# Performance work log

Hardware: AMD Instinct MI355X
Metric: run time of the kernel (lower is better)

## Reference

```python
import jax, jax.numpy as jnp
import numpy as np

H = 4          # num attention heads
LRELU = 0.2    # DGL GATConv leaky-relu slope
N_GT, N_AG = 100000, 20000
E_GT, E_COMM = 640000, 320000
D_GT, D_AG = 32, 64
VIS, COMM, MSG, OUT = 64, 128, 64, 5
NUM_COMM_STEPS = 2


def _leaky(x):
    return jnp.where(x >= 0, x, LRELU * x)


def gat(feat_src, feat_dst, w_src, w_dst, a_l, a_r, bias, src, dst, n_dst, dh):
    """Bipartite DGL GATConv: residual=Identity (in_dst == H*dh), activation=ReLU."""
    fs = (feat_src @ w_src).reshape(-1, H, dh)   # [Ns,H,dh]
    fd = (feat_dst @ w_dst).reshape(-1, H, dh)   # [Nd,H,dh]
    el = (fs * a_l[None]).sum(-1)                # [Ns,H]
    er = (fd * a_r[None]).sum(-1)                # [Nd,H]
    e = _leaky(el[src] + er[dst])                # [E,H]
    emax = jax.ops.segment_max(e, dst, num_segments=n_dst)
    ex = jnp.exp(e - emax[dst])
    denom = jax.ops.segment_sum(ex, dst, num_segments=n_dst)
    a = ex / denom[dst]                          # edge softmax over in-edges
    rst = jax.ops.segment_sum(fs[src] * a[..., None], dst, num_segments=n_dst)
    rst = rst + feat_dst.reshape(n_dst, H, dh)   # identity residual
    rst = rst + bias.reshape(1, H, dh)
    return jax.nn.relu(rst).reshape(n_dst, H * dh)


def gru(x, h, w_ih, w_hh, b_ih, b_hh):
    gi = x @ w_ih + b_ih
    gh = h @ w_hh + b_hh
    i_r, i_z, i_n = jnp.split(gi, 3, axis=1)
    h_r, h_z, h_n = jnp.split(gh, 3, axis=1)
    r = jax.nn.sigmoid(i_r + h_r)
    zg = jax.nn.sigmoid(i_z + h_z)
    n = jnp.tanh(i_n + r * h_n)
    return (1.0 - zg) * n + zg * h


def setup_inputs() -> dict:
    key = jax.random.key(0)
    ks = jax.random.split(key, 32)
    def w(k, shp):
        return (jax.random.normal(k, shp, dtype=jnp.float32) / np.sqrt(shp[0])).astype(jnp.float32)
    dh1, dh2 = VIS // H, COMM // H
    inp = {
        'feat_gt': jax.random.normal(ks[0], (N_GT, D_GT), dtype=jnp.float32),
        'feat_agent': jax.random.normal(ks[1], (N_AG, D_AG), dtype=jnp.float32),
        'z': jax.random.normal(ks[2], (N_AG, COMM), dtype=jnp.float32),
        'gt_src': jax.random.randint(ks[3], (E_GT,), 0, N_GT, dtype=jnp.int32),
        'gt_dst': jax.random.randint(ks[4], (E_GT,), 0, N_AG, dtype=jnp.int32),
        'comm_src': jax.random.randint(ks[5], (E_COMM,), 0, N_AG, dtype=jnp.int32),
        'comm_dst': jax.random.randint(ks[6], (E_COMM,), 0, N_AG, dtype=jnp.int32),
        # vis1 GATConv (gt->agent), out 64 = 4 heads x 16
        'w1_src': w(ks[7], (D_GT, VIS)), 'w1_dst': w(ks[8], (D_AG, VIS)),
        'a1_l': w(ks[9], (H, dh1)), 'a1_r': w(ks[10], (H, dh1)),
        'b1': jnp.zeros((VIS,), jnp.float32),
        'w2_src': w(ks[11], (D_GT, COMM)), 'w2_dst': w(ks[12], (VIS + D_AG, COMM)),
        'a2_l': w(ks[13], (H, dh2)), 'a2_r': w(ks[14], (H, dh2)),
        'b2': jnp.zeros((COMM,), jnp.float32),
        # comm f_enc: mlp([128,128,64]) with ReLU everywhere
        'enc_w1': w(ks[15], (COMM, 128)), 'enc_b1': jnp.zeros((128,), jnp.float32),
        'enc_w2': w(ks[16], (128, MSG)), 'enc_b2': jnp.zeros((MSG,), jnp.float32),
        # GRUCell(in=COMM+MSG=192, hidden=COMM=128), stored [in, 3*hidden]
        'gru_w_ih': w(ks[17], (COMM + MSG, 3 * COMM)),
        'gru_w_hh': w(ks[18], (COMM, 3 * COMM)),
        'gru_b_ih': jnp.zeros((3 * COMM,), jnp.float32),
        'gru_b_hh': jnp.zeros((3 * COMM,), jnp.float32),
        # f_out
        'out_w': w(ks[19], (COMM, OUT)), 'out_b': jnp.zeros((OUT,), jnp.float32),
    }
    return inp


def _forward(feat_gt, feat_agent, z, gt_src, gt_dst, comm_src, comm_dst,
             w1_src, w1_dst, a1_l, a1_r, b1,
             w2_src, w2_dst, a2_l, a2_r, b2,
             enc_w1, enc_b1, enc_w2, enc_b2,
             gru_w_ih, gru_w_hh, gru_b_ih, gru_b_hh,
             out_w, out_b):
    n_ag = feat_agent.shape[0]
    h_vis1 = gat(feat_gt, feat_agent, w1_src, w1_dst, a1_l, a1_r, b1,
                 gt_src, gt_dst, n_ag, VIS // H)
    dst2 = jnp.concatenate([h_vis1, feat_agent], axis=1)
    h = gat(feat_gt, dst2, w2_src, w2_dst, a2_l, a2_r, b2,
            gt_src, gt_dst, n_ag, COMM // H)
    deg = jax.ops.segment_sum(jnp.ones_like(comm_dst, dtype=jnp.float32),
                              comm_dst, num_segments=n_ag)
    denom = jnp.maximum(deg, 1.0)[:, None]
    zz = z
    for _ in range(NUM_COMM_STEPS):
        m = jax.nn.relu(jax.nn.relu(h @ enc_w1 + enc_b1) @ enc_w2 + enc_b2)  # per-node f_enc
        y = jax.ops.segment_sum(m[comm_src], comm_dst, num_segments=n_ag) / denom  # mailbox mean
        h = gru(jnp.concatenate([h, y], axis=1), zz, gru_w_ih, gru_w_hh, gru_b_ih, gru_b_hh)
        zz = h
    h_out = h @ out_w + out_b
    return h_out, zz


def reference(feat_gt, feat_agent, z, gt_src, gt_dst, comm_src, comm_dst,
              w1_src, w1_dst, a1_l, a1_r, b1,
              w2_src, w2_dst, a2_l, a2_r, b2,
              enc_w1, enc_b1, enc_w2, enc_b2,
              gru_w_ih, gru_w_hh, gru_b_ih, gru_b_hh,
              out_w, out_b):
    return _forward(feat_gt, feat_agent, z, gt_src, gt_dst, comm_src, comm_dst,
                    w1_src, w1_dst, a1_l, a1_r, b1,
                    w2_src, w2_dst, a2_l, a2_r, b2,
                    enc_w1, enc_b1, enc_w2, enc_b2,
                    gru_w_ih, gru_w_hh, gru_b_ih, gru_b_hh,
                    out_w, out_b)
```

## Files before the change

### kernel.cpp

```cpp
#include <hip/hip_runtime.h>
#include <math.h>

#define NHEAD 4
#define LRELU_S 0.2f
constexpr int N_GT = 100000, N_AG = 20000;
constexpr int E_GT = 640000, E_COMM = 320000;
constexpr int OUTD = 5;
constexpr int NBLK_SC = (N_AG + 255) / 256;
constexpr int MB_GT = (N_GT + 63) / 64;
constexpr int FS_TILES = 3 * MB_GT;
constexpr int ETILES  = (N_AG + 31) / 32;
constexpr int GGROUPS = (N_AG + 3) / 4;

constexpr long O_CNTP_GT = 0;
constexpr long O_CNTP_CM = 320000;
constexpr long O_FSB1    = 0;
constexpr long O_FSB2    = 3200000;
constexpr long O_EL1     = 12800000;
constexpr long O_EL2     = 13200000;
constexpr long O_ER1     = 14880000;
constexpr long O_RST2    = 17600000;
constexpr long O_DINV    = 20160000;
constexpr long O_OFFS_GT = 20180000;
constexpr long O_SRT_GT  = 20200004;
constexpr long O_OFFS_CM = 20840004;
constexpr long O_SRT_CM  = 20860008;
constexpr long O_PART    = 21180008;
constexpr long O_V       = 21220008;
constexpr long O_WB      = 21300000;
constexpr long O_RANK_GT = 21500000;
constexpr long O_RANK_CM = 22140000;
constexpr long O_M  = 10240000;

constexpr long WB_FS  = 0;
constexpr long WB_E1  = 6144;
constexpr long WB_E2  = 22528;
constexpr long WB_RZ  = 30720;
constexpr long WB_GIN = 112640;
constexpr long WB_GHN = 137216;

using bf8      = __attribute__((ext_vector_type(8))) short;
using f32x4v   = __attribute__((ext_vector_type(4))) float;
using ushort8v = __attribute__((ext_vector_type(8))) unsigned short;

__device__ __forceinline__ unsigned short f2bf(float x) {
    unsigned u = __float_as_uint(x);
    u += 0x7FFFu + ((u >> 16) & 1u);
    return (unsigned short)(u >> 16);
}
__device__ __forceinline__ float bf2f(unsigned short u) {
    return __uint_as_float(((unsigned)u) << 16);
}

__global__ __launch_bounds__(256) void p0_k(
    const float* __restrict__ w1s, const float* __restrict__ w1d,
    const float* __restrict__ a1l, const float* __restrict__ a1r,
    const float* __restrict__ w2s, const float* __restrict__ w2d,
    const float* __restrict__ a2l, const float* __restrict__ a2r,
    const float* __restrict__ e1, const float* __restrict__ e2,
    const float* __restrict__ gih, const float* __restrict__ ghh,
    float* __restrict__ ws)
{
    const int tid = (int)(blockIdx.x * 256 + threadIdx.x);
    const int NT  = (int)(gridDim.x * 256);
    unsigned* wsu = reinterpret_cast<unsigned*>(ws);
    unsigned short* wb = reinterpret_cast<unsigned short*>(ws + O_WB);
    for (int i = tid; i < 640000; i += NT) wsu[O_CNTP_GT + i] = 0u;
    for (int i = tid; i < 153600; i += NT) {
        float val;
        if (i < 2048)        { long l = i;          long n = l / 32,  k = l % 32;  val = w1s[k * 64 + n]; }
        else if (i < 6144)   { long l = i - 2048;   long n = l / 32,  k = l % 32;  val = w2s[k * 128 + n]; }
        else if (i < 22528)  { long l = i - 6144;   long n = l / 128, k = l % 128; val = e1[k * 128 + n]; }
        else if (i < 30720)  { long l = i - 22528;  long n = l / 128, k = l % 128; val = e2[k * 64 + n]; }
        else if (i < 112640) { long l = i - 30720;  long n = l / 320, k = l % 320;
                               val = (k < 192) ? gih[k * 384 + n] : ghh[(k - 192) * 384 + n]; }
        else if (i < 137216) { long l = i - 112640; long n = l / 192, k = l % 192; val = gih[k * 384 + 256 + n]; }
        else                 { long l = i - 137216; long n = l / 128, k = l % 128; val = ghh[k * 384 + 256 + n]; }
        wb[i] = f2bf(val);
    }
    if (tid < 1024) {
        const int i = tid;
        const float *wp, *ap; int dh, local;
        if (i < 128)      { wp = w1s; ap = a1l; dh = 16; local = i; }
        else if (i < 384) { wp = w1d; ap = a1r; dh = 16; local = i - 128; }
        else if (i < 512) { wp = w2s; ap = a2l; dh = 32; local = i - 384; }
        else              { wp = w2d; ap = a2r; dh = 32; local = i - 512; }
        int k = local >> 2, hh = local & 3;
        float s = 0.f;
        for (int j = 0; j < dh; ++j) s += wp[k * (4 * dh) + hh * dh + j] * ap[hh * dh + j];
        ws[O_V + i] = s;
    }
}

__global__ __launch_bounds__(256) void p1_k(
    const int* __restrict__ gt_dst, const int* __restrict__ comm_dst,
    const float* __restrict__ feat_gt, const float* __restrict__ feat_agent,
    float* __restrict__ ws)
{
    const int tid = (int)(blockIdx.x * 256 + threadIdx.x);
    unsigned* wsu = reinterpret_cast<unsigned*>(ws);
    if (tid < E_GT) {
        wsu[O_RANK_GT + tid] = atomicAdd(wsu + O_CNTP_GT + (long)gt_dst[tid] * 16, 1u);
    } else if (tid < E_GT + E_COMM) {
        int j = tid - E_GT;
        wsu[O_RANK_CM + j] = atomicAdd(wsu + O_CNTP_CM + (long)comm_dst[j] * 16, 1u);
    }
    const float* v1  = ws + O_V;
    const float* v2  = ws + O_V + 384;
    const float* vr1 = ws + O_V + 128;
    float* el1 = ws + O_EL1;
    float* el2 = ws + O_EL2;
    float* er1 = ws + O_ER1;
    if (tid < N_GT) {
        const int i = tid;
        float a[8] = {};
        const float* fp = feat_gt + (long)i * 32;
        for (int k = 0; k < 32; ++k) {
            float x = fp[k];
#pragma unroll
            for (int j = 0; j < 4; ++j) a[j] += x * v1[4 * k + j];
#pragma unroll
            for (int j = 0; j < 4; ++j) a[4 + j] += x * v2[4 * k + j];
        }
        *reinterpret_cast<float4*>(el1 + 4l * i) = {a[0], a[1], a[2], a[3]};
        *reinterpret_cast<float4*>(el2 + 4l * i) = {a[4], a[5], a[6], a[7]};
    } else if (tid < N_GT + N_AG) {
        int r = tid - N_GT;
        float a0 = 0, a1 = 0, a2 = 0, a3 = 0;
        const float* fp = feat_agent + (long)r * 64;
        for (int k = 0; k < 64; ++k) {
            float x = fp[k];
            a0 += x * vr1[4 * k];     a1 += x * vr1[4 * k + 1];
            a2 += x * vr1[4 * k + 2]; a3 += x * vr1[4 * k + 3];
        }
        *reinterpret_cast<float4*>(er1 + 4l * r) = {a0, a1, a2, a3};
    }
}

__global__ __launch_bounds__(256) void p2_k(float* __restrict__ ws)
{
    __shared__ unsigned shu[256];
    unsigned* wsu = reinterpret_cast<unsigned*>(ws);
    const int b = (int)blockIdx.x, t = (int)threadIdx.x;
    const int g  = (b >= NBLK_SC) ? 1 : 0;
    const int cb = b - g * NBLK_SC;
    const int i  = cb * 256 + t;
    const unsigned* cnt = wsu + (g ? O_CNTP_CM : O_CNTP_GT);
    unsigned c = (i < N_AG) ? cnt[(long)i * 16] : 0u;
    if (g && i < N_AG) ws[O_DINV + i] = 1.0f / fmaxf((float)c, 1.0f);
    shu[t] = c;
    __syncthreads();
    for (int off = 1; off < 256; off <<= 1) {
        unsigned v = (t >= off) ? shu[t - off] : 0u;
        __syncthreads();
        shu[t] += v;
        __syncthreads();
    }
    unsigned* offs = wsu + (g ? O_OFFS_CM : O_OFFS_GT);
    if (i < N_AG) offs[i] = shu[t] - c;
    if (t == 255) wsu[O_PART + b] = shu[255];
}

__global__ __launch_bounds__(256) void p3_k(float* __restrict__ ws)
{
    __shared__ unsigned shu[128];
    unsigned* wsu = reinterpret_cast<unsigned*>(ws);
    const int b = (int)blockIdx.x, t = (int)threadIdx.x;
    const int g  = (b >= NBLK_SC) ? 1 : 0;
    const int cb = b - g * NBLK_SC;
    if (t < 128) shu[t] = (t < cb) ? wsu[O_PART + g * NBLK_SC + t] : 0u;
    __syncthreads();
    for (int off = 64; off >= 1; off >>= 1) {
        if (t < off) shu[t] += shu[t + off];
        __syncthreads();
    }
    const unsigned pre = shu[0];
    unsigned* offs = wsu + (g ? O_OFFS_CM : O_OFFS_GT);
    const int i = cb * 256 + t;
    if (i < N_AG) offs[i] += pre;
    if (b == NBLK_SC - 1 && t == 0)     wsu[O_OFFS_GT + N_AG] = E_GT;
    if (b == 2 * NBLK_SC - 1 && t == 0) wsu[O_OFFS_CM + N_AG] = E_COMM;
}

__global__ __launch_bounds__(256) void p4_k(
    const int* __restrict__ gt_src, const int* __restrict__ gt_dst,
    const int* __restrict__ comm_src, const int* __restrict__ comm_dst,
    const float* __restrict__ A, float* __restrict__ ws)
{
    unsigned* wsu = reinterpret_cast<unsigned*>(ws);
    const int t = (int)threadIdx.x;
    const int tid = (int)(blockIdx.x * 256 + t);
    if (tid < E_GT) {
        wsu[O_SRT_GT + wsu[O_OFFS_GT + gt_dst[tid]] + wsu[O_RANK_GT + tid]] = (unsigned)gt_src[tid];
    } else if (tid < E_GT + E_COMM) {
        int j = tid - E_GT;
        wsu[O_SRT_CM + wsu[O_OFFS_CM + comm_dst[j]] + wsu[O_RANK_CM + j]] = (unsigned)comm_src[j];
    }

    __shared__ __align__(16) unsigned short As[64][40];
    __shared__ __align__(16) unsigned short Bs[64][40];
    const unsigned short* Btc = reinterpret_cast<unsigned short*>(ws + O_WB) + WB_FS;
    unsigned short* fsb1 = reinterpret_cast<unsigned short*>(ws + O_FSB1);
    unsigned short* fsb2 = reinterpret_cast<unsigned short*>(ws + O_FSB2);
    const int lane = t & 63, wv = t >> 6;
    const int wm = wv & 1, wn = wv >> 1;
    const int quad = lane >> 4, l16 = lane & 15;
    const int rA = t >> 3, cA = (t & 7) * 4;
    const int rB = t >> 2, cB = (t & 3) * 8;
    const int tt = (int)blockIdx.x;
    if (tt >= FS_TILES) return;
    const int n0 = (tt % 3) * 64, m0 = (tt / 3) * 64;
#pragma unroll
    for (int half = 0; half < 2; ++half) {
        const int r = rA + half * 32;
        const int row = m0 + r;
        float4 v = {0.f, 0.f, 0.f, 0.f};
        if (row < N_GT) v = *reinterpret_cast<const float4*>(A + (long)row * 32 + cA);
        ushort4 bb;
        bb.x = f2bf(v.x); bb.y = f2bf(v.y); bb.z = f2bf(v.z); bb.w = f2bf(v.w);
        *reinterpret_cast<ushort4*>(&As[r][cA]) = bb;
    }
    *reinterpret_cast<ushort8v*>(&Bs[rB][cB]) =
        *reinterpret_cast<const ushort8v*>(Btc + (long)(n0 + rB) * 32 + cB);
    __syncthreads();
    f32x4v acc[2][2] = {};
    const bf8 a0 = *reinterpret_cast<const bf8*>(&As[wm * 32 + l16][quad * 8]);
    const bf8 a1 = *reinterpret_cast<const bf8*>(&As[wm * 32 + 16 + l16][quad * 8]);
    const bf8 b0v = *reinterpret_cast<const bf8*>(&Bs[wn * 32 + l16][quad * 8]);
    const bf8 b1v = *reinterpret_cast<const bf8*>(&Bs[wn * 32 + 16 + l16][quad * 8]);
    acc[0][0] = __builtin_amdgcn_mfma_f32_16x16x32_bf16(a0, b0v, acc[0][0], 0, 0, 0);
    acc[0][1] = __builtin_amdgcn_mfma_f32_16x16x32_bf16(a0, b1v, acc[0][1], 0, 0, 0);
    acc[1][0] = __builtin_amdgcn_mfma_f32_16x16x32_bf16(a1, b0v, acc[1][0], 0, 0, 0);
    acc[1][1] = __builtin_amdgcn_mfma_f32_16x16x32_bf16(a1, b1v, acc[1][1], 0, 0, 0);
#pragma unroll
    for (int mt = 0; mt < 2; ++mt)
#pragma unroll
        for (int nt = 0; nt < 2; ++nt)
#pragma unroll
            for (int r = 0; r < 4; ++r) {
                const int row = m0 + wm * 32 + mt * 16 + quad * 4 + r;
                const int col = n0 + wn * 32 + nt * 16 + l16;
                if (row < N_GT) {
                    unsigned short v16 = f2bf(acc[mt][nt][r]);
                    if (col < 64) fsb1[(long)row * 64 + col] = v16;
                    else          fsb2[(long)row * 128 + (col - 64)] = v16;
                }
            }
}

__global__ __launch_bounds__(256) void gat12_k(
    const unsigned* __restrict__ offs, const unsigned* __restrict__ ssrc,
    const float* __restrict__ el1, const float* __restrict__ er1,
    const float* __restrict__ el2,
    const unsigned short* __restrict__ fsb1, const unsigned short* __restrict__ fsb2,
    const float* __restrict__ feat_agent,
    const float* __restrict__ b1, const float* __restrict__ b2,
    const float* __restrict__ vr2, float* __restrict__ out)
{
    const int wid = threadIdx.x >> 6, lane = threadIdx.x & 63;
    const int d = blockIdx.x * 4 + wid;
    if (d >= N_AG) return;
    const int h = lane >> 4, ei = lane & 15;
    const unsigned beg = __builtin_amdgcn_readfirstlane(offs[d]);
    const unsigned end = __builtin_amdgcn_readfirstlane(offs[d + 1]);
    const unsigned smax = (unsigned)N_GT - 1u;

    float s = 0.f, acc0 = 0.f;
    {
        const float er_h = er1[4l * d + h];
        for (unsigned base = beg; base < end; base += 16) {
            const unsigned na = min(16u, end - base);
            unsigned sv = ssrc[base + ((unsigned)ei < na ? (unsigned)ei : 0u)];
            sv = min(sv, smax);
            float p = 0.f;
            if ((unsigned)ei < na) {
                float x = el1[4l * sv + h] + er_h;
                x = (x >= 0.f) ? x : LRELU_S * x;
                p = __expf(x);
            }
            unsigned short fw[16];
#pragma unroll
            for (int j = 0; j < 16; ++j) {
                const unsigned sj = min(ssrc[min(base + (unsigned)j, end - 1u)], smax);
                fw[j] = fsb1[(long)sj * 64 + lane];
            }
#pragma unroll
            for (int j = 0; j < 16; ++j) {
                const float pj = __shfl(p, (h << 4) | j);
                s += pj;
                acc0 += pj * bf2f(fw[j]);
            }
        }
    }
    const float inv1 = (s > 0.f) ? 1.f / s : 0.f;
    const float r1 = feat_agent[(long)d * 64 + lane];
    const float o = fmaxf(acc0 * inv1 + r1 + b1[lane], 0.f);

    float e0 = o * vr2[lane * 4 + 0] + r1 * vr2[(64 + lane) * 4 + 0];
    float e1v = o * vr2[lane * 4 + 1] + r1 * vr2[(64 + lane) * 4 + 1];
    float e2v = o * vr2[lane * 4 + 2] + r1 * vr2[(64 + lane) * 4 + 2];
    float e3v = o * vr2[lane * 4 + 3] + r1 * vr2[(64 + lane) * 4 + 3];
#pragma unroll
    for (int off = 1; off < 64; off <<= 1) {
        e0  += __shfl_xor(e0, off);
        e1v += __shfl_xor(e1v, off);
        e2v += __shfl_xor(e2v, off);
        e3v += __shfl_xor(e3v, off);
    }
    const float er_h2 = (h == 0) ? e0 : (h == 1) ? e1v : (h == 2) ? e2v : e3v;

    const int c0 = lane * 2;
    float s2 = 0.f, A0 = 0.f, A1 = 0.f;
    for (unsigned base = beg; base < end; base += 16) {
        const unsigned na = min(16u, end - base);
        unsigned sv = ssrc[base + ((unsigned)ei < na ? (unsigned)ei : 0u)];
        sv = min(sv, smax);
        float p = 0.f;
        if ((unsigned)ei < na) {
            float x = el2[4l * sv + h] + er_h2;
            x = (x >= 0.f) ? x : LRELU_S * x;
            p = __expf(x);
        }
        unsigned fw[16];
#pragma unroll
        for (int j = 0; j < 16; ++j) {
            const unsigned sj = min(ssrc[min(base + (unsigned)j, end - 1u)], smax);
            fw[j] = *reinterpret_cast<const unsigned*>(fsb2 + (long)sj * 128 + c0);
        }
#pragma unroll
        for (int j = 0; j < 16; ++j) {
            const float pj = __shfl(p, (h << 4) | j);
            s2 += pj;
            A0 += pj * __uint_as_float((fw[j] & 0xFFFFu) << 16);
            A1 += pj * __uint_as_float((fw[j] >> 16) << 16);
        }
    }
    const float inv2 = (s2 > 0.f) ? 1.f / s2 : 0.f;
    const float rox = __shfl(o, c0 & 63);
    const float roy = __shfl(o, (c0 + 1) & 63);
    float2 r;
    if (c0 < 64) { r.x = rox; r.y = roy; }
    else r = *reinterpret_cast<const float2*>(feat_agent + (long)d * 64 + (c0 - 64));
    float2 oo;
    oo.x = fmaxf(A0 * inv2 + r.x + b2[c0], 0.f);
    oo.y = fmaxf(A1 * inv2 + r.y + b2[c0 + 1], 0.f);
    *reinterpret_cast<float2*>(out + (long)d * 128 + c0) = oo;
}

__global__ __launch_bounds__(512) void enc_k(
    const float* __restrict__ h,
    const unsigned short* __restrict__ we1, const unsigned short* __restrict__ we2,
    const float* __restrict__ eb1, const float* __restrict__ eb2,
    unsigned short* __restrict__ mb)
{
    __shared__ __align__(16) unsigned short As[32][136];
    __shared__ __align__(16) unsigned short Ts[32][136];
    const int tid = (int)threadIdx.x;
    const int lane = tid & 63, w = tid >> 6;
    const int quad = lane >> 4, l16 = lane & 15;
    const int m0 = (int)blockIdx.x * 32;
#pragma unroll
    for (int it = 0; it < 2; ++it) {
        int idx = tid + it * 512;
        int row = idx >> 5, cc = (idx & 31) * 4;
        int grow = m0 + row;
        float4 v = {0.f, 0.f, 0.f, 0.f};
        if (grow < N_AG) v = *reinterpret_cast<const float4*>(h + (long)grow * 128 + cc);
        ushort4 b;
        b.x = f2bf(v.x); b.y = f2bf(v.y); b.z = f2bf(v.z); b.w = f2bf(v.w);
        *reinterpret_cast<ushort4*>(&As[row][cc]) = b;
    }
    __syncthreads();
    {
        const int j0 = w * 16;
        const unsigned short* p = we1 + (long)(j0 + l16) * 128 + quad * 8;
        bf8 bw[4];
#pragma unroll
        for (int i = 0; i < 4; ++i) bw[i] = *reinterpret_cast<const bf8*>(p + i * 32);
        f32x4v acc[2] = {};
#pragma unroll
        for (int i = 0; i < 4; ++i) {
            const int k0 = i * 32;
            const bf8 a0 = *reinterpret_cast<const bf8*>(&As[l16][k0 + quad * 8]);
            const bf8 a1 = *reinterpret_cast<const bf8*>(&As[16 + l16][k0 + quad * 8]);
            acc[0] = __builtin_amdgcn_mfma_f32_16x16x32_bf16(a0, bw[i], acc[0], 0, 0, 0);
            acc[1] = __builtin_amdgcn_mfma_f32_16x16x32_bf16(a1, bw[i], acc[1], 0, 0, 0);
        }
        const int j = j0 + l16;
        const float bj = eb1[j];
#pragma unroll
        for (int mt = 0; mt < 2; ++mt)
#pragma unroll
            for (int r = 0; r < 4; ++r)
                Ts[mt * 16 + quad * 4 + r][j] = f2bf(fmaxf(acc[mt][r] + bj, 0.f));
    }
    __syncthreads();
    if (w < 4) {
        const int j0 = w * 16;
        const unsigned short* p = we2 + (long)(j0 + l16) * 128 + quad * 8;
        bf8 bw[4];
#pragma unroll
        for (int i = 0; i < 4; ++i) bw[i] = *reinterpret_cast<const bf8*>(p + i * 32);
        f32x4v acc[2] = {};
#pragma unroll
        for (int i = 0; i < 4; ++i) {
            const int k0 = i * 32;
            const bf8 a0 = *reinterpret_cast<const bf8*>(&Ts[l16][k0 + quad * 8]);
            const bf8 a1 = *reinterpret_cast<const bf8*>(&Ts[16 + l16][k0 + quad * 8]);
            acc[0] = __builtin_amdgcn_mfma_f32_16x16x32_bf16(a0, bw[i], acc[0], 0, 0, 0);
            acc[1] = __builtin_amdgcn_mfma_f32_16x16x32_bf16(a1, bw[i], acc[1], 0, 0, 0);
        }
        const int j = j0 + l16;
        const float bj = eb2[j];
#pragma unroll
        for (int mt = 0; mt < 2; ++mt)
#pragma unroll
            for (int r = 0; r < 4; ++r) {
                const int row = m0 + mt * 16 + quad * 4 + r;
                if (row < N_AG)
                    mb[(long)row * 64 + j] = f2bf(fmaxf(acc[mt][r] + bj, 0.f));
            }
    }
}

__global__ __launch_bounds__(512) void gru_k(
    const float* __restrict__ h_in,
    const unsigned* __restrict__ coffs, const unsigned* __restrict__ cssrc,
    const unsigned short* __restrict__ mbx, const float* __restrict__ dinv,
    const float* zz,
    const unsigned short* __restrict__ wrz, const unsigned short* __restrict__ wgin,
    const unsigned short* __restrict__ wghn,
    const float* __restrict__ gbih, const float* __restrict__ gbhh,
    float* hout,
    const float* __restrict__ ow, const float* __restrict__ ob, float* __restrict__ outp)
{
    __shared__ __align__(16) unsigned short As[32][328];
    __shared__ __align__(16) float Ys[32][64];
    const int tid = (int)threadIdx.x;
    const int lane = tid & 63, w = tid >> 6;
    const int quad = lane >> 4, l16 = lane & 15;
    const int m0 = (int)blockIdx.x * 32;

    {
        const unsigned smax = (unsigned)N_AG - 1u;
#pragma unroll 1
        for (int q = 0; q < 4; ++q) {
            const int d = m0 + w * 4 + q;
            const unsigned beg  = __builtin_amdgcn_readfirstlane(coffs[d]);
            const unsigned endo = __builtin_amdgcn_readfirstlane(coffs[d + 1]);
            float acc = 0.f;
            for (unsigned base = beg; base < endo; base += 32) {
                const unsigned na = min(32u, endo - base);
                unsigned short fw[32];
#pragma unroll
                for (int j = 0; j < 32; ++j) {
                    const unsigned sj = min(cssrc[min(base + (unsigned)j, endo - 1u)], smax);
                    fw[j] = mbx[(long)sj * 64 + lane];
                }
#pragma unroll
                for (int j = 0; j < 32; ++j)
                    if ((unsigned)j < na) acc += bf2f(fw[j]);
            }
            Ys[w * 4 + q][lane] = acc * dinv[d];
        }
    }
    __syncthreads();

#pragma unroll
    for (int it = 0; it < 5; ++it) {
        int idx = tid + it * 512;
        int row = idx / 80, cc = (idx - row * 80) * 4;
        int grow = m0 + row;
        float4 v = {0.f, 0.f, 0.f, 0.f};
        if (grow < N_AG) {
            if (cc < 128)      v = *reinterpret_cast<const float4*>(h_in + (long)grow * 128 + cc);
            else if (cc < 192) v = *reinterpret_cast<const float4*>(&Ys[row][cc - 128]);
            else               v = *reinterpret_cast<const float4*>(zz + (long)grow * 128 + (cc - 192));
        }
        ushort4 b;
        b.x = f2bf(v.x); b.y = f2bf(v.y); b.z = f2bf(v.z); b.w = f2bf(v.w);
        *reinterpret_cast<ushort4*>(&As[row][cc]) = b;
    }
    __syncthreads();

    f32x4v aR[2] = {}, aZ[2] = {}, aI[2] = {}, aH[2] = {};
    const int j0 = w * 16;
    const unsigned short* pR = wrz + (long)(j0 + l16) * 320 + quad * 8;
    const unsigned short* pZ = wrz + (long)(128 + j0 + l16) * 320 + quad * 8;
#pragma unroll
    for (int half = 0; half < 2; ++half) {
        bf8 bR[5], bZ[5];
#pragma unroll
        for (int i = 0; i < 5; ++i) {
            const int k0 = half * 160 + i * 32;
            bR[i] = *reinterpret_cast<const bf8*>(pR + k0);
            bZ[i] = *reinterpret_cast<const bf8*>(pZ + k0);
        }
#pragma unroll
        for (int i = 0; i < 5; ++i) {
            const int k0 = half * 160 + i * 32;
            const bf8 a0 = *reinterpret_cast<const bf8*>(&As[l16][k0 + quad * 8]);
            const bf8 a1 = *reinterpret_cast<const bf8*>(&As[16 + l16][k0 + quad * 8]);
            aR[0] = __builtin_amdgcn_mfma_f32_16x16x32_bf16(a0, bR[i], aR[0], 0, 0, 0);
            aR[1] = __builtin_amdgcn_mfma_f32_16x16x32_bf16(a1, bR[i], aR[1], 0, 0, 0);
            aZ[0] = __builtin_amdgcn_mfma_f32_16x16x32_bf16(a0, bZ[i], aZ[0], 0, 0, 0);
            aZ[1] = __builtin_amdgcn_mfma_f32_16x16x32_bf16(a1, bZ[i], aZ[1], 0, 0, 0);
        }
    }
    {
        const unsigned short* pI = wgin + (long)(j0 + l16) * 192 + quad * 8;
        bf8 bI[6];
#pragma unroll
        for (int i = 0; i < 6; ++i) bI[i] = *reinterpret_cast<const bf8*>(pI + i * 32);
#pragma unroll
        for (int i = 0; i < 6; ++i) {
            const int k0 = i * 32;
            const bf8 a0 = *reinterpret_cast<const bf8*>(&As[l16][k0 + quad * 8]);
            const bf8 a1 = *reinterpret_cast<const bf8*>(&As[16 + l16][k0 + quad * 8]);
            aI[0] = __builtin_amdgcn_mfma_f32_16x16x32_bf16(a0, bI[i], aI[0], 0, 0, 0);
            aI[1] = __builtin_amdgcn_mfma_f32_16x16x32_bf16(a1, bI[i], aI[1], 0, 0, 0);
        }
    }
    {
        const unsigned short* pH = wghn + (long)(j0 + l16) * 128 + quad * 8;
        bf8 bH[4];
#pragma unroll
        for (int i = 0; i < 4; ++i) bH[i] = *reinterpret_cast<const bf8*>(pH + i * 32);
#pragma unroll
        for (int i = 0; i < 4; ++i) {
            const int k0 = 192 + i * 32;
            const bf8 a0 = *reinterpret_cast<const bf8*>(&As[l16][k0 + quad * 8]);
            const bf8 a1 = *reinterpret_cast<const bf8*>(&As[16 + l16][k0 + quad * 8]);
            aH[0] = __builtin_amdgcn_mfma_f32_16x16x32_bf16(a0, bH[i], aH[0], 0, 0, 0);
            aH[1] = __builtin_amdgcn_mfma_f32_16x16x32_bf16(a1, bH[i], aH[1], 0, 0, 0);
        }
    }
    const int j = j0 + l16;
    float hv[2][4];
#pragma unroll
    for (int mt = 0; mt < 2; ++mt)
#pragma unroll
        for (int r = 0; r < 4; ++r) {
            const int row = m0 + mt * 16 + quad * 4 + r;
            float v = 0.f;
            if (row < N_AG) {
                const float rr = 1.f / (1.f + __expf(-(aR[mt][r] + gbih[j] + gbhh[j])));
                const float zg = 1.f / (1.f + __expf(-(aZ[mt][r] + gbih[128 + j] + gbhh[128 + j])));
                const float nn = tanhf(aI[mt][r] + gbih[256 + j] + rr * (aH[mt][r] + gbhh[256 + j]));
                const float hp = zz[(long)row * 128 + j];
                v = (1.f - zg) * nn + zg * hp;
            }
            hv[mt][r] = v;
        }

    if (outp == nullptr) {
#pragma unroll
        for (int mt = 0; mt < 2; ++mt)
#pragma unroll
            for (int r = 0; r < 4; ++r) {
                const int row = m0 + mt * 16 + quad * 4 + r;
                if (row < N_AG) hout[(long)row * 128 + j] = hv[mt][r];
            }
    } else {
        __syncthreads();
        float* Hs = reinterpret_cast<float*>(&As[0][0]);
#pragma unroll
        for (int mt = 0; mt < 2; ++mt)
#pragma unroll
            for (int r = 0; r < 4; ++r)
                Hs[(mt * 16 + quad * 4 + r) * 128 + j] = hv[mt][r];
        __syncthreads();
        for (int it = tid; it < 32 * 32; it += 512) {
            const int row = it >> 5, c4 = (it & 31) * 4;
            const float4 v = *reinterpret_cast<const float4*>(&Hs[row * 128 + c4]);
            *reinterpret_cast<float4*>(outp + (long)N_AG * OUTD + (long)(m0 + row) * 128 + c4) = v;
        }
        for (int it = tid; it < 32 * OUTD; it += 512) {
            const int row = it / OUTD, jj = it - row * OUTD;
            float a = ob[jj];
            const float* hr = &Hs[row * 128];
            for (int k = 0; k < 128; ++k) a += hr[k] * ow[k * OUTD + jj];
            outp[(long)(m0 + row) * OUTD + jj] = a;
        }
    }
}

extern "C" void kernel_launch(void* const* d_in, const int* in_sizes, int n_in,
                              void* d_out, int out_size, void* d_ws, size_t ws_size,
                              hipStream_t stream) {
    const float* feat_gt    = (const float*)d_in[0];
    const float* feat_agent = (const float*)d_in[1];
    const float* z_in       = (const float*)d_in[2];
    const int*   gt_src     = (const int*)d_in[3];
    const int*   gt_dst     = (const int*)d_in[4];
    const int*   comm_src   = (const int*)d_in[5];
    const int*   comm_dst   = (const int*)d_in[6];
    const float* w1_src = (const float*)d_in[7];
    const float* w1_dst = (const float*)d_in[8];
    const float* a1_l   = (const float*)d_in[9];
    const float* a1_r   = (const float*)d_in[10];
    const float* b1     = (const float*)d_in[11];
    const float* w2_src = (const float*)d_in[12];
    const float* w2_dst = (const float*)d_in[13];
    const float* a2_l   = (const float*)d_in[14];
    const float* a2_r   = (const float*)d_in[15];
    const float* b2     = (const float*)d_in[16];
    const float* enc_w1 = (const float*)d_in[17];
    const float* enc_b1 = (const float*)d_in[18];
    const float* enc_w2 = (const float*)d_in[19];
    const float* enc_b2 = (const float*)d_in[20];
    const float* gw_ih  = (const float*)d_in[21];
    const float* gw_hh  = (const float*)d_in[22];
    const float* gb_ih  = (const float*)d_in[23];
    const float* gb_hh  = (const float*)d_in[24];
    const float* out_w  = (const float*)d_in[25];
    const float* out_b  = (const float*)d_in[26];

    float* ws = (float*)d_ws;
    unsigned* wsu = (unsigned*)d_ws;
    unsigned short* wb = (unsigned short*)(ws + O_WB);
    float* out = (float*)d_out;

    float* hptr = ws + O_RST2;
    unsigned short* mb = (unsigned short*)(ws + O_M);

    p0_k<<<dim3(2500), dim3(256), 0, stream>>>(w1_src, w1_dst, a1_l, a1_r,
                                               w2_src, w2_dst, a2_l, a2_r,
                                               enc_w1, enc_w2, gw_ih, gw_hh, ws);
    p1_k<<<dim3(3750), dim3(256), 0, stream>>>(gt_dst, comm_dst, feat_gt, feat_agent, ws);
    p2_k<<<dim3(2 * NBLK_SC), dim3(256), 0, stream>>>(ws);
    p3_k<<<dim3(2 * NBLK_SC), dim3(256), 0, stream>>>(ws);
    p4_k<<<dim3(FS_TILES), dim3(256), 0, stream>>>(gt_src, gt_dst, comm_src, comm_dst,
                                                   feat_gt, ws);

    gat12_k<<<dim3(GGROUPS), dim3(256), 0, stream>>>(
        wsu + O_OFFS_GT, wsu + O_SRT_GT,
        ws + O_EL1, ws + O_ER1, ws + O_EL2,
        (const unsigned short*)(ws + O_FSB1), (const unsigned short*)(ws + O_FSB2),
        feat_agent, b1, b2, ws + O_V + 512, hptr);

    for (int step = 0; step < 2; ++step) {
        const float* zz = (step == 0) ? z_in : hptr;
        enc_k<<<dim3(ETILES), dim3(512), 0, stream>>>(hptr, wb + WB_E1, wb + WB_E2,
                                                      enc_b1, enc_b2, mb);
        gru_k<<<dim3(ETILES), dim3(512), 0, stream>>>(hptr,
                                                      wsu + O_OFFS_CM, wsu + O_SRT_CM,
                                                      mb, ws + O_DINV, zz,
                                                      wb + WB_RZ, wb + WB_GIN, wb + WB_GHN,
                                                      gb_ih, gb_hh, hptr,
                                                      (step == 1) ? out_w : nullptr,
                                                      (step == 1) ? out_b : nullptr,
                                                      (step == 1) ? out : nullptr);
    }
}
```

Before: 362.6 us.

## Fuse scan kernels and give each fs GEMM block all three column tiles

The two-pass block scan (p2/p3) becomes a single kernel in which each block recomputes its prefix by summing all earlier counts directly, which removes one launch and the partial-sum buffer. The scatter/GEMM kernel p4 now launches one block per 64-row tile and loops over all three 64-column output tiles. The A tile is loaded once instead of three times, and the edge scatter becomes a grid-stride loop. In exchange, each scan block re-reads up to N_AG strided counts, and p4 runs a third as many blocks with more serial work per block.

```diff
diff --git a/kernel.cpp b/kernel.cpp
--- a/kernel.cpp
+++ b/kernel.cpp
@@ -8,7 +8,6 @@
 constexpr int OUTD = 5;
 constexpr int NBLK_SC = (N_AG + 255) / 256;
 constexpr int MB_GT = (N_GT + 63) / 64;
-constexpr int FS_TILES = 3 * MB_GT;
 constexpr int ETILES  = (N_AG + 31) / 32;
 constexpr int GGROUPS = (N_AG + 3) / 4;
 
@@ -137,15 +136,27 @@
     }
 }
 
-__global__ __launch_bounds__(256) void p2_k(float* __restrict__ ws)
+__global__ __launch_bounds__(256) void p23_k(float* __restrict__ ws)
 {
     __shared__ unsigned shu[256];
     unsigned* wsu = reinterpret_cast<unsigned*>(ws);
     const int b = (int)blockIdx.x, t = (int)threadIdx.x;
     const int g  = (b >= NBLK_SC) ? 1 : 0;
     const int cb = b - g * NBLK_SC;
-    const int i  = cb * 256 + t;
     const unsigned* cnt = wsu + (g ? O_CNTP_CM : O_CNTP_GT);
+
+    unsigned psum = 0u;
+    for (int i = t; i < cb * 256; i += 256) psum += cnt[(long)i * 16];
+    shu[t] = psum;
+    __syncthreads();
+    for (int off = 128; off >= 1; off >>= 1) {
+        if (t < off) shu[t] += shu[t + off];
+        __syncthreads();
+    }
+    const unsigned pre = shu[0];
+    __syncthreads();
+
+    const int i = cb * 256 + t;
     unsigned c = (i < N_AG) ? cnt[(long)i * 16] : 0u;
     if (g && i < N_AG) ws[O_DINV + i] = 1.0f / fmaxf((float)c, 1.0f);
     shu[t] = c;
@@ -157,27 +168,7 @@
         __syncthreads();
     }
     unsigned* offs = wsu + (g ? O_OFFS_CM : O_OFFS_GT);
-    if (i < N_AG) offs[i] = shu[t] - c;
-    if (t == 255) wsu[O_PART + b] = shu[255];
-}
-
-__global__ __launch_bounds__(256) void p3_k(float* __restrict__ ws)
-{
-    __shared__ unsigned shu[128];
-    unsigned* wsu = reinterpret_cast<unsigned*>(ws);
-    const int b = (int)blockIdx.x, t = (int)threadIdx.x;
-    const int g  = (b >= NBLK_SC) ? 1 : 0;
-    const int cb = b - g * NBLK_SC;
-    if (t < 128) shu[t] = (t < cb) ? wsu[O_PART + g * NBLK_SC + t] : 0u;
-    __syncthreads();
-    for (int off = 64; off >= 1; off >>= 1) {
-        if (t < off) shu[t] += shu[t + off];
-        __syncthreads();
-    }
-    const unsigned pre = shu[0];
-    unsigned* offs = wsu + (g ? O_OFFS_CM : O_OFFS_GT);
-    const int i = cb * 256 + t;
-    if (i < N_AG) offs[i] += pre;
+    if (i < N_AG) offs[i] = pre + shu[t] - c;
     if (b == NBLK_SC - 1 && t == 0)     wsu[O_OFFS_GT + N_AG] = E_GT;
     if (b == 2 * NBLK_SC - 1 && t == 0) wsu[O_OFFS_CM + N_AG] = E_COMM;
 }
@@ -189,16 +180,18 @@
 {
     unsigned* wsu = reinterpret_cast<unsigned*>(ws);
     const int t = (int)threadIdx.x;
-    const int tid = (int)(blockIdx.x * 256 + t);
-    if (tid < E_GT) {
-        wsu[O_SRT_GT + wsu[O_OFFS_GT + gt_dst[tid]] + wsu[O_RANK_GT + tid]] = (unsigned)gt_src[tid];
-    } else if (tid < E_GT + E_COMM) {
-        int j = tid - E_GT;
-        wsu[O_SRT_CM + wsu[O_OFFS_CM + comm_dst[j]] + wsu[O_RANK_CM + j]] = (unsigned)comm_src[j];
+    const int NT = (int)(gridDim.x * 256);
+    for (int i = (int)(blockIdx.x * 256 + t); i < E_GT + E_COMM; i += NT) {
+        if (i < E_GT) {
+            wsu[O_SRT_GT + wsu[O_OFFS_GT + gt_dst[i]] + wsu[O_RANK_GT + i]] = (unsigned)gt_src[i];
+        } else {
+            int j = i - E_GT;
+            wsu[O_SRT_CM + wsu[O_OFFS_CM + comm_dst[j]] + wsu[O_RANK_CM + j]] = (unsigned)comm_src[j];
+        }
     }
 
     __shared__ __align__(16) unsigned short As[64][40];
-    __shared__ __align__(16) unsigned short Bs[64][40];
+    __shared__ __align__(16) unsigned short Bs[192][40];
     const unsigned short* Btc = reinterpret_cast<unsigned short*>(ws + O_WB) + WB_FS;
     unsigned short* fsb1 = reinterpret_cast<unsigned short*>(ws + O_FSB1);
     unsigned short* fsb2 = reinterpret_cast<unsigned short*>(ws + O_FSB2);
@@ -206,10 +199,7 @@
     const int wm = wv & 1, wn = wv >> 1;
     const int quad = lane >> 4, l16 = lane & 15;
     const int rA = t >> 3, cA = (t & 7) * 4;
-    const int rB = t >> 2, cB = (t & 3) * 8;
-    const int tt = (int)blockIdx.x;
-    if (tt >= FS_TILES) return;
-    const int n0 = (tt % 3) * 64, m0 = (tt / 3) * 64;
+    const int m0 = (int)blockIdx.x * 64;
 #pragma unroll
     for (int half = 0; half < 2; ++half) {
         const int r = rA + half * 32;
@@ -220,32 +210,41 @@
         bb.x = f2bf(v.x); bb.y = f2bf(v.y); bb.z = f2bf(v.z); bb.w = f2bf(v.w);
         *reinterpret_cast<ushort4*>(&As[r][cA]) = bb;
     }
-    *reinterpret_cast<ushort8v*>(&Bs[rB][cB]) =
-        *reinterpret_cast<const ushort8v*>(Btc + (long)(n0 + rB) * 32 + cB);
-    __syncthreads();
-    f32x4v acc[2][2] = {};
+#pragma unroll
+    for (int it = 0; it < 3; ++it) {
+        const int idx = t + it * 256;
+        const int r = idx >> 2, c8 = (idx & 3) * 8;
+        *reinterpret_cast<ushort8v*>(&Bs[r][c8]) =
+            *reinterpret_cast<const ushort8v*>(Btc + (long)r * 32 + c8);
+    }
+    __syncthreads();
     const bf8 a0 = *reinterpret_cast<const bf8*>(&As[wm * 32 + l16][quad * 8]);
     const bf8 a1 = *reinterpret_cast<const bf8*>(&As[wm * 32 + 16 + l16][quad * 8]);
-    const bf8 b0v = *reinterpret_cast<const bf8*>(&Bs[wn * 32 + l16][quad * 8]);
-    const bf8 b1v = *reinterpret_cast<const bf8*>(&Bs[wn * 32 + 16 + l16][quad * 8]);
-    acc[0][0] = __builtin_amdgcn_mfma_f32_16x16x32_bf16(a0, b0v, acc[0][0], 0, 0, 0);
-    acc[0][1] = __builtin_amdgcn_mfma_f32_16x16x32_bf16(a0, b1v, acc[0][1], 0, 0, 0);
-    acc[1][0] = __builtin_amdgcn_mfma_f32_16x16x32_bf16(a1, b0v, acc[1][0], 0, 0, 0);
-    acc[1][1] = __builtin_amdgcn_mfma_f32_16x16x32_bf16(a1, b1v, acc[1][1], 0, 0, 0);
-#pragma unroll
-    for (int mt = 0; mt < 2; ++mt)
-#pragma unroll
-        for (int nt = 0; nt < 2; ++nt)
-#pragma unroll
-            for (int r = 0; r < 4; ++r) {
-                const int row = m0 + wm * 32 + mt * 16 + quad * 4 + r;
-                const int col = n0 + wn * 32 + nt * 16 + l16;
-                if (row < N_GT) {
-                    unsigned short v16 = f2bf(acc[mt][nt][r]);
-                    if (col < 64) fsb1[(long)row * 64 + col] = v16;
-                    else          fsb2[(long)row * 128 + (col - 64)] = v16;
+#pragma unroll
+    for (int q = 0; q < 3; ++q) {
+        const int n0 = q * 64;
+        f32x4v acc[2][2] = {};
+        const bf8 b0v = *reinterpret_cast<const bf8*>(&Bs[n0 + wn * 32 + l16][quad * 8]);
+        const bf8 b1v = *reinterpret_cast<const bf8*>(&Bs[n0 + wn * 32 + 16 + l16][quad * 8]);
+        acc[0][0] = __builtin_amdgcn_mfma_f32_16x16x32_bf16(a0, b0v, acc[0][0], 0, 0, 0);
+        acc[0][1] = __builtin_amdgcn_mfma_f32_16x16x32_bf16(a0, b1v, acc[0][1], 0, 0, 0);
+        acc[1][0] = __builtin_amdgcn_mfma_f32_16x16x32_bf16(a1, b0v, acc[1][0], 0, 0, 0);
+        acc[1][1] = __builtin_amdgcn_mfma_f32_16x16x32_bf16(a1, b1v, acc[1][1], 0, 0, 0);
+#pragma unroll
+        for (int mt = 0; mt < 2; ++mt)
+#pragma unroll
+            for (int nt = 0; nt < 2; ++nt)
+#pragma unroll
+                for (int r = 0; r < 4; ++r) {
+                    const int row = m0 + wm * 32 + mt * 16 + quad * 4 + r;
+                    const int col = n0 + wn * 32 + nt * 16 + l16;
+                    if (row < N_GT) {
+                        unsigned short v16 = f2bf(acc[mt][nt][r]);
+                        if (col < 64) fsb1[(long)row * 64 + col] = v16;
+                        else          fsb2[(long)row * 128 + (col - 64)] = v16;
+                    }
                 }
-            }
+    }
 }
 
 __global__ __launch_bounds__(256) void gat12_k(
@@ -628,10 +627,9 @@
                                                w2_src, w2_dst, a2_l, a2_r,
                                                enc_w1, enc_w2, gw_ih, gw_hh, ws);
     p1_k<<<dim3(3750), dim3(256), 0, stream>>>(gt_dst, comm_dst, feat_gt, feat_agent, ws);
-    p2_k<<<dim3(2 * NBLK_SC), dim3(256), 0, stream>>>(ws);
-    p3_k<<<dim3(2 * NBLK_SC), dim3(256), 0, stream>>>(ws);
-    p4_k<<<dim3(FS_TILES), dim3(256), 0, stream>>>(gt_src, gt_dst, comm_src, comm_dst,
-                                                   feat_gt, ws);
+    p23_k<<<dim3(2 * NBLK_SC), dim3(256), 0, stream>>>(ws);
+    p4_k<<<dim3(MB_GT), dim3(256), 0, stream>>>(gt_src, gt_dst, comm_src, comm_dst,
+                                                feat_gt, ws);
 
     gat12_k<<<dim3(GGROUPS), dim3(256), 0, stream>>>(
         wsu + O_OFFS_GT, wsu + O_SRT_GT,
```

Result: no change. 369.7 us (+2.0%).
